# Kernel tuning notes

Hardware: AMD Instinct MI355X
Metric: run time of the kernel (lower is better)

The kernel has to match this reference:

```python
import jax, jax.numpy as jnp
import numpy as np

N_NODES = 50000
N_EDGES = 800000
D_IN = 128
D_OUT = 128


def setup_inputs() -> dict:
    key = jax.random.key(0)
    k_feat, k_src, k_dst, k_ws, k_bs, k_wn = jax.random.split(key, 6)
    feat = jax.random.normal(k_feat, (N_NODES, D_IN), dtype=jnp.float32)
    src = jax.random.randint(k_src, (N_EDGES,), 0, N_NODES, dtype=jnp.int64)
    dst = jax.random.randint(k_dst, (N_EDGES,), 0, N_NODES, dtype=jnp.int64)
    # fc_self: Linear(D_IN, D_OUT, bias=True); fc_neigh: Linear(D_IN, D_OUT, bias=False)
    W_self = jax.random.normal(k_ws, (D_OUT, D_IN), dtype=jnp.float32) * (1.0 / np.sqrt(D_IN))
    b_self = jax.random.normal(k_bs, (D_OUT,), dtype=jnp.float32) * 0.01
    # xavier_uniform with relu gain
    gain = float(np.sqrt(2.0))
    bound = gain * float(np.sqrt(6.0 / (D_IN + D_OUT)))
    W_neigh = jax.random.uniform(k_wn, (D_OUT, D_IN), dtype=jnp.float32, minval=-bound, maxval=bound)
    bias = jnp.zeros((D_OUT,), dtype=jnp.float32)
    return {"feat": feat, "src": src, "dst": dst, "W_self": W_self,
            "b_self": b_self, "W_neigh": W_neigh, "bias": bias}


def reference(feat, src, dst, W_self, b_self, W_neigh, bias):
    # copy_u('h','m') + fn.mean('m','neigh'): gather src feats, mean-reduce by dst.
    # lin_before_mp is False (in_feats == out_feats), so aggregate raw feats first.
    n = feat.shape[0]
    msgs = feat[src]                                             # [E, D_IN]
    neigh_sum = jax.ops.segment_sum(msgs, dst, num_segments=n)   # [N, D_IN]
    deg = jax.ops.segment_sum(jnp.ones(src.shape, feat.dtype), dst, num_segments=n)
    # DGL mean yields 0 for zero-in-degree nodes
    h_neigh = jnp.where(deg[:, None] > 0, neigh_sum / jnp.maximum(deg, 1.0)[:, None], 0.0)
    h_neigh = h_neigh @ W_neigh.T                                # fc_neigh (no bias)
    h_self = feat @ W_self.T + b_self                            # fc_self
    return h_self + h_neigh + bias
```

## Files before the change

kernel.cpp:

```cpp
#include <hip/hip_runtime.h>
#include <hip/hip_fp8.h>

#define N_NODES 50000
#define N_EDGES 800000
#define D 128
#define NBUK 196
#define CAPR 4591
#define CAPP 6400
#define PCHUNK 4096
#define PBLOCKS 196

typedef __bf16 bf16x8 __attribute__((ext_vector_type(8)));
typedef __bf16 bf16x4 __attribute__((ext_vector_type(4)));
typedef float  f32x4  __attribute__((ext_vector_type(4)));
typedef float  f32x2  __attribute__((ext_vector_type(2)));

#if defined(__has_builtin)
#if __has_builtin(__builtin_amdgcn_cvt_pk_f32_fp8) && __has_builtin(__builtin_amdgcn_cvt_pk_fp8_f32)
#define HW_FP8 1
#endif
#endif

#define OFF_GCURSOR   0ull
#define OFF_OFFS      1024ull
#define OFF_PACKED    201216ull
#define OFF_FEAT8     5218816ull
#define OFF_WC16      11618944ull
#define OFF_BIASC     11684480ull

__global__ __launch_bounds__(256)
void partition_kernel(const int* __restrict__ src, const int* __restrict__ dst,
                      int* __restrict__ gcursor, int* __restrict__ packed, int n) {
    __shared__ int lh[NBUK];
    __shared__ int lbase[NBUK];
    const int tid = threadIdx.x;
    const int e0 = blockIdx.x * PCHUNK;
    int d[16], s[16];
    for (int i = tid; i < NBUK; i += 256) lh[i] = 0;
    __syncthreads();
    #pragma unroll
    for (int j = 0; j < 16; ++j) {
        int e = e0 + j * 256 + tid;
        bool ok = e < n;
        d[j] = ok ? dst[e] : -1;
        s[j] = ok ? src[e] : 0;
        if (ok) atomicAdd(&lh[d[j] >> 8], 1);
    }
    __syncthreads();
    for (int i = tid; i < NBUK; i += 256) {
        int c = lh[i];
        lbase[i] = c ? atomicAdd(&gcursor[i], c) : 0;
    }
    __syncthreads();
    for (int i = tid; i < NBUK; i += 256) lh[i] = 0;
    __syncthreads();
    #pragma unroll
    for (int j = 0; j < 16; ++j) {
        if (d[j] >= 0) {
            int b = d[j] >> 8;
            int r = atomicAdd(&lh[b], 1);
            int pos = lbase[b] + r;
            if (pos < CAPR)
                packed[b * CAPP + pos] = ((d[j] & 255) << 16) | s[j];
        }
    }
}

__global__ __launch_bounds__(256)
void mix_kernel(int* __restrict__ packed, const int* __restrict__ gcursor,
                int* __restrict__ offs,
                const float* __restrict__ feat, unsigned char* __restrict__ feat8,
                const float* __restrict__ Ws, const float* __restrict__ Wn,
                const float* __restrict__ b_self, const float* __restrict__ bias,
                __bf16* __restrict__ Wc16, float* __restrict__ biasc) {
    __shared__ int pk[CAPR];
    __shared__ int srt[CAPP];
    __shared__ int lh[256];
    __shared__ int loff[256];
    __shared__ int ws5[5];
    const int tid = threadIdx.x;
    if (blockIdx.x < NBUK) {
        const int lane = tid & 63;
        const int wv = tid >> 6;
        const int b = blockIdx.x;
        const int node0 = b * 256;
        const int ncnt = min(256, N_NODES - node0);
        const int base = b * CAPP;
        const int cnt = min(gcursor[b], CAPR);

        for (int i = tid; i < cnt; i += 256) pk[i] = packed[base + i];
        lh[tid] = 0;
        __syncthreads();
        for (int i = tid; i < cnt; i += 256)
            atomicAdd(&lh[pk[i] >> 16], 1);
        __syncthreads();
        int c  = lh[tid];
        int cp = (c + 7) & ~7;
        int v = cp;
        #pragma unroll
        for (int o = 1; o < 64; o <<= 1) {
            int u = __shfl_up(v, o);
            if (lane >= o) v += u;
        }
        if (lane == 63) ws5[wv] = v;
        __syncthreads();
        if (tid == 0) {
            int r = 0;
            #pragma unroll
            for (int j = 0; j < 4; ++j) { int t = ws5[j]; ws5[j] = r; r += t; }
            ws5[4] = r;
        }
        __syncthreads();
        int ex = ws5[wv] + (v - cp);
        loff[tid] = ex;
        lh[tid] = 0;
        __syncthreads();
        for (int i = tid; i < cnt; i += 256) {
            int p = pk[i];
            int l = p >> 16;
            int r = atomicAdd(&lh[l], 1);
            srt[loff[l] + r] = p & 0xFFFF;
        }
        for (int j = c; j < cp; ++j) srt[ex + j] = N_NODES;
        __syncthreads();
        const int ptot = ws5[4];
        for (int i = tid; i < ptot; i += 256) packed[base + i] = srt[i];
        if (tid < ncnt) offs[node0 + tid] = (ex << 16) | c;
    } else if (blockIdx.x < NBUK + 3125) {
        size_t i = ((size_t)(blockIdx.x - NBUK) * 256 + tid) * 8;
        float4 f0 = *(const float4*)(feat + i);
        float4 f1 = *(const float4*)(feat + i + 4);
#ifdef HW_FP8
        int q0 = __builtin_amdgcn_cvt_pk_fp8_f32(f0.x, f0.y, 0, false);
        q0     = __builtin_amdgcn_cvt_pk_fp8_f32(f0.z, f0.w, q0, true);
        int q1 = __builtin_amdgcn_cvt_pk_fp8_f32(f1.x, f1.y, 0, false);
        q1     = __builtin_amdgcn_cvt_pk_fp8_f32(f1.z, f1.w, q1, true);
        uint2 qq; qq.x = (unsigned)q0; qq.y = (unsigned)q1;
        *(uint2*)(feat8 + i) = qq;
#else
        float fv[8] = {f0.x, f0.y, f0.z, f0.w, f1.x, f1.y, f1.z, f1.w};
        union { unsigned char b[8]; unsigned long long u; } q;
        #pragma unroll
        for (int j = 0; j < 8; ++j) { __hip_fp8_e4m3 e(fv[j]); q.b[j] = e.__x; }
        *(unsigned long long*)(feat8 + i) = q.u;
#endif
    } else if (blockIdx.x < NBUK + 3157) {
        int idx = (blockIdx.x - NBUK - 3125) * 256 + tid;
        int col = idx >> 6;
        int kq  = (idx & 63) * 4;
        const float* srcp = (kq < D) ? (Ws + (size_t)col * D + kq)
                                     : (Wn + (size_t)col * D + (kq - D));
        float4 f = *(const float4*)srcp;
        bf16x4 t;
        t[0]=(__bf16)f.x; t[1]=(__bf16)f.y; t[2]=(__bf16)f.z; t[3]=(__bf16)f.w;
        *(bf16x4*)(Wc16 + (size_t)col * 256 + kq) = t;
    } else {
        if (tid < D) biasc[tid] = b_self[tid] + bias[tid];
        else if (tid < D + 32)
            ((unsigned*)(feat8 + (size_t)N_NODES * D))[tid - 128] = 0u;
    }
}

__device__ __forceinline__
void gemm_tail(__bf16 (*At)[264], const __bf16* __restrict__ Wc16,
               const float* __restrict__ biasc, float* __restrict__ out,
               int node0, int tid) {
    const int wv = tid >> 6;
    const int lane = tid & 63;
    const int m = lane & 15;
    const int quad = lane >> 4;
    const int r0 = (wv & 1) * 32;
    const int c0 = (wv >> 1) * 64;

    f32x4 acc[2][4] = {};
    #pragma unroll
    for (int k0 = 0; k0 < 256; k0 += 32) {
        const int kk = k0 + quad * 8;
        bf16x8 a0 = *(const bf16x8*)&At[r0 + m][kk];
        bf16x8 a1 = *(const bf16x8*)&At[r0 + 16 + m][kk];
        #pragma unroll
        for (int ct = 0; ct < 4; ++ct) {
            int col = c0 + ct * 16 + m;
            bf16x8 b = *(const bf16x8*)(Wc16 + (size_t)col * 256 + kk);
            acc[0][ct] = __builtin_amdgcn_mfma_f32_16x16x32_bf16(a0, b, acc[0][ct], 0, 0, 0);
            acc[1][ct] = __builtin_amdgcn_mfma_f32_16x16x32_bf16(a1, b, acc[1][ct], 0, 0, 0);
        }
    }
    __syncthreads();

    float* Ct = (float*)&At[0][0];
    #pragma unroll
    for (int rt = 0; rt < 2; ++rt) {
        #pragma unroll
        for (int ct = 0; ct < 4; ++ct) {
            int ccol = c0 + ct * 16 + m;
            int crow = r0 + rt * 16 + quad * 4;
            #pragma unroll
            for (int r = 0; r < 4; ++r)
                Ct[(crow + r) * 132 + ccol] = acc[rt][ct][r];
        }
    }
    __syncthreads();
    for (int idx = tid; idx < 64 * 32; idx += 256) {
        int row = idx >> 5;
        int c4 = (idx & 31) * 4;
        int n = node0 + row;
        if (n < N_NODES) {
            float4 v = *(float4*)&Ct[row * 132 + c4];
            float4 bb = *(const float4*)(biasc + c4);
            v.x += bb.x; v.y += bb.y; v.z += bb.z; v.w += bb.w;
            *(float4*)&out[(size_t)n * D + c4] = v;
        }
    }
}

__device__ __forceinline__ float fp8tof_sw(unsigned char b) {
    __hip_fp8_e4m3 t; t.__x = b;
    return (float)t;
}

__global__ __launch_bounds__(256)
void fused_kernel(const float* __restrict__ feat,
                  const unsigned char* __restrict__ feat8,
                  const int* __restrict__ offs,
                  const int* __restrict__ csr,
                  const __bf16* __restrict__ Wc16,
                  const float* __restrict__ biasc,
                  float* __restrict__ out) {
    __shared__ __bf16 At[64][264];
    const int tid = threadIdx.x;
    const int node0 = blockIdx.x * 64;

    for (int idx = tid; idx < 1024; idx += 256) {
        int row = idx >> 4;
        int seg = (idx & 15) * 8;
        int n = node0 + row;
        bf16x8 t = {};
        if (n < N_NODES) {
            const float* p = feat + (size_t)n * D + seg;
            float4 f0 = *(const float4*)p;
            float4 f1 = *(const float4*)(p + 4);
            t[0]=(__bf16)f0.x; t[1]=(__bf16)f0.y; t[2]=(__bf16)f0.z; t[3]=(__bf16)f0.w;
            t[4]=(__bf16)f1.x; t[5]=(__bf16)f1.y; t[6]=(__bf16)f1.z; t[7]=(__bf16)f1.w;
        }
        *(bf16x8*)&At[row][seg] = t;
    }

    {
        const int hw = tid >> 5;
        const int lane = tid & 31;
        const unsigned int* g8 = (const unsigned int*)feat8;
        int ovs[8];
        #pragma unroll
        for (int t = 0; t < 8; ++t) {
            int n = node0 + hw + t * 8;
            ovs[t] = (n < N_NODES) ? offs[n] : 0;
        }
        #pragma unroll
        for (int t = 0; t < 8; ++t) {
            int i = hw + t * 8;
            int n = node0 + i;
            int dg = ovs[t] & 0xFFFF;
            int dgp = (dg + 7) & ~7;
            float a0 = 0.f, a1 = 0.f, a2 = 0.f, a3 = 0.f;
            if (n < N_NODES && dg > 0) {
                const int* lst = csr + (n >> 8) * CAPP + (ovs[t] >> 16);
                for (int j = 0; j < dgp; j += 8) {
                    int s[8]; unsigned int w[8];
                    #pragma unroll
                    for (int q = 0; q < 8; ++q) s[q] = lst[j + q];
                    #pragma unroll
                    for (int q = 0; q < 8; ++q)
                        w[q] = g8[(size_t)s[q] * 32 + lane];
                    #pragma unroll
                    for (int q = 0; q < 8; ++q) {
#ifdef HW_FP8
                        f32x2 lo = __builtin_amdgcn_cvt_pk_f32_fp8((int)w[q], false);
                        f32x2 hi = __builtin_amdgcn_cvt_pk_f32_fp8((int)w[q], true);
                        a0 += lo[0]; a1 += lo[1]; a2 += hi[0]; a3 += hi[1];
#else
                        a0 += fp8tof_sw(w[q] & 0xFF);
                        a1 += fp8tof_sw((w[q] >> 8) & 0xFF);
                        a2 += fp8tof_sw((w[q] >> 16) & 0xFF);
                        a3 += fp8tof_sw(w[q] >> 24);
#endif
                    }
                }
            }
            float sc = dg > 0 ? 1.0f / (float)dg : 0.f;
            bf16x4 hv;
            hv[0] = (__bf16)(a0 * sc); hv[1] = (__bf16)(a1 * sc);
            hv[2] = (__bf16)(a2 * sc); hv[3] = (__bf16)(a3 * sc);
            *(bf16x4*)&At[i][128 + lane * 4] = hv;
        }
    }
    __syncthreads();
    gemm_tail(At, Wc16, biasc, out, node0, tid);
}

extern "C" void kernel_launch(void* const* d_in, const int* in_sizes, int n_in,
                              void* d_out, int out_size, void* d_ws, size_t ws_size,
                              hipStream_t stream) {
    const float* feat    = (const float*)d_in[0];
    const int*   src     = (const int*)d_in[1];
    const int*   dst     = (const int*)d_in[2];
    const float* W_self  = (const float*)d_in[3];
    const float* b_self  = (const float*)d_in[4];
    const float* W_neigh = (const float*)d_in[5];
    const float* bias    = (const float*)d_in[6];
    float* out = (float*)d_out;
    char*  ws  = (char*)d_ws;

    int* gcursor = (int*)(ws + OFF_GCURSOR);
    int* offs    = (int*)(ws + OFF_OFFS);
    int* packed  = (int*)(ws + OFF_PACKED);
    unsigned char* feat8 = (unsigned char*)(ws + OFF_FEAT8);
    __bf16* Wc16 = (__bf16*)(ws + OFF_WC16);
    float* biasc = (float*)(ws + OFF_BIASC);
    const int n_edges = in_sizes[1];

    hipMemsetAsync(gcursor, 0, 1024, stream);
    partition_kernel<<<dim3(PBLOCKS), 256, 0, stream>>>(src, dst, gcursor, packed, n_edges);
    mix_kernel<<<dim3(NBUK + 3158), 256, 0, stream>>>(packed, gcursor, offs,
                                                      feat, feat8, W_self, W_neigh,
                                                      b_self, bias, Wc16, biasc);
    fused_kernel<<<dim3((N_NODES + 63) / 64), 256, 0, stream>>>(
        feat, feat8, offs, packed, Wc16, biasc, out);
}
```

Baseline: 147.1 us.

## Move fp8/weight prep into partition kernel and split gather across half-waves

The fp8 feature quantization and weight/bias packing now run in the same launch as the edge partition, and the local CSR sort becomes its own small kernel. The goal is to overlap the bandwidth-heavy conversion with the atomic-bound partition and keep the sort kernel light on shared memory so it occupies the GPU better. In the gather, each full wave now handles one node, with the two half-waves taking alternate neighbours. Neighbour indices are read as int4 vectors, 16 per iteration, and the two halves are combined with a cross-lane shuffle. This gives more memory parallelism per node but spends half the lanes idle on the write-back and adds shuffles.

```diff
diff --git a/kernel.cpp b/kernel.cpp
--- a/kernel.cpp
+++ b/kernel.cpp
@@ -29,105 +29,48 @@
 #define OFF_BIASC     11684480ull
 
 __global__ __launch_bounds__(256)
-void partition_kernel(const int* __restrict__ src, const int* __restrict__ dst,
-                      int* __restrict__ gcursor, int* __restrict__ packed, int n) {
+void prep_kernel(const int* __restrict__ src, const int* __restrict__ dst,
+                 int* __restrict__ gcursor, int* __restrict__ packed, int n,
+                 const float* __restrict__ feat, unsigned char* __restrict__ feat8,
+                 const float* __restrict__ Ws, const float* __restrict__ Wn,
+                 const float* __restrict__ b_self, const float* __restrict__ bias,
+                 __bf16* __restrict__ Wc16, float* __restrict__ biasc) {
     __shared__ int lh[NBUK];
     __shared__ int lbase[NBUK];
     const int tid = threadIdx.x;
-    const int e0 = blockIdx.x * PCHUNK;
-    int d[16], s[16];
-    for (int i = tid; i < NBUK; i += 256) lh[i] = 0;
-    __syncthreads();
-    #pragma unroll
-    for (int j = 0; j < 16; ++j) {
-        int e = e0 + j * 256 + tid;
-        bool ok = e < n;
-        d[j] = ok ? dst[e] : -1;
-        s[j] = ok ? src[e] : 0;
-        if (ok) atomicAdd(&lh[d[j] >> 8], 1);
-    }
-    __syncthreads();
-    for (int i = tid; i < NBUK; i += 256) {
-        int c = lh[i];
-        lbase[i] = c ? atomicAdd(&gcursor[i], c) : 0;
-    }
-    __syncthreads();
-    for (int i = tid; i < NBUK; i += 256) lh[i] = 0;
-    __syncthreads();
-    #pragma unroll
-    for (int j = 0; j < 16; ++j) {
-        if (d[j] >= 0) {
-            int b = d[j] >> 8;
-            int r = atomicAdd(&lh[b], 1);
-            int pos = lbase[b] + r;
-            if (pos < CAPR)
-                packed[b * CAPP + pos] = ((d[j] & 255) << 16) | s[j];
-        }
-    }
-}
-
-__global__ __launch_bounds__(256)
-void mix_kernel(int* __restrict__ packed, const int* __restrict__ gcursor,
-                int* __restrict__ offs,
-                const float* __restrict__ feat, unsigned char* __restrict__ feat8,
-                const float* __restrict__ Ws, const float* __restrict__ Wn,
-                const float* __restrict__ b_self, const float* __restrict__ bias,
-                __bf16* __restrict__ Wc16, float* __restrict__ biasc) {
-    __shared__ int pk[CAPR];
-    __shared__ int srt[CAPP];
-    __shared__ int lh[256];
-    __shared__ int loff[256];
-    __shared__ int ws5[5];
-    const int tid = threadIdx.x;
-    if (blockIdx.x < NBUK) {
-        const int lane = tid & 63;
-        const int wv = tid >> 6;
-        const int b = blockIdx.x;
-        const int node0 = b * 256;
-        const int ncnt = min(256, N_NODES - node0);
-        const int base = b * CAPP;
-        const int cnt = min(gcursor[b], CAPR);
-
-        for (int i = tid; i < cnt; i += 256) pk[i] = packed[base + i];
-        lh[tid] = 0;
+    if (blockIdx.x < PBLOCKS) {
+        const int e0 = blockIdx.x * PCHUNK;
+        int d[16], s[16];
+        for (int i = tid; i < NBUK; i += 256) lh[i] = 0;
         __syncthreads();
-        for (int i = tid; i < cnt; i += 256)
-            atomicAdd(&lh[pk[i] >> 16], 1);
+        #pragma unroll
+        for (int j = 0; j < 16; ++j) {
+            int e = e0 + j * 256 + tid;
+            bool ok = e < n;
+            d[j] = ok ? dst[e] : -1;
+            s[j] = ok ? src[e] : 0;
+            if (ok) atomicAdd(&lh[d[j] >> 8], 1);
+        }
         __syncthreads();
-        int c  = lh[tid];
-        int cp = (c + 7) & ~7;
-        int v = cp;
-        #pragma unroll
-        for (int o = 1; o < 64; o <<= 1) {
-            int u = __shfl_up(v, o);
-            if (lane >= o) v += u;
-        }
-        if (lane == 63) ws5[wv] = v;
+        for (int i = tid; i < NBUK; i += 256) {
+            int c = lh[i];
+            lbase[i] = c ? atomicAdd(&gcursor[i], c) : 0;
+        }
         __syncthreads();
-        if (tid == 0) {
-            int r = 0;
-            #pragma unroll
-            for (int j = 0; j < 4; ++j) { int t = ws5[j]; ws5[j] = r; r += t; }
-            ws5[4] = r;
-        }
+        for (int i = tid; i < NBUK; i += 256) lh[i] = 0;
         __syncthreads();
-        int ex = ws5[wv] + (v - cp);
-        loff[tid] = ex;
-        lh[tid] = 0;
-        __syncthreads();
-        for (int i = tid; i < cnt; i += 256) {
-            int p = pk[i];
-            int l = p >> 16;
-            int r = atomicAdd(&lh[l], 1);
-            srt[loff[l] + r] = p & 0xFFFF;
-        }
-        for (int j = c; j < cp; ++j) srt[ex + j] = N_NODES;
-        __syncthreads();
-        const int ptot = ws5[4];
-        for (int i = tid; i < ptot; i += 256) packed[base + i] = srt[i];
-        if (tid < ncnt) offs[node0 + tid] = (ex << 16) | c;
-    } else if (blockIdx.x < NBUK + 3125) {
-        size_t i = ((size_t)(blockIdx.x - NBUK) * 256 + tid) * 8;
+        #pragma unroll
+        for (int j = 0; j < 16; ++j) {
+            if (d[j] >= 0) {
+                int b = d[j] >> 8;
+                int r = atomicAdd(&lh[b], 1);
+                int pos = lbase[b] + r;
+                if (pos < CAPR)
+                    packed[b * CAPP + pos] = ((d[j] & 255) << 16) | s[j];
+            }
+        }
+    } else if (blockIdx.x < PBLOCKS + 3125) {
+        size_t i = ((size_t)(blockIdx.x - PBLOCKS) * 256 + tid) * 8;
         float4 f0 = *(const float4*)(feat + i);
         float4 f1 = *(const float4*)(feat + i + 4);
 #ifdef HW_FP8
@@ -144,8 +87,8 @@
         for (int j = 0; j < 8; ++j) { __hip_fp8_e4m3 e(fv[j]); q.b[j] = e.__x; }
         *(unsigned long long*)(feat8 + i) = q.u;
 #endif
-    } else if (blockIdx.x < NBUK + 3157) {
-        int idx = (blockIdx.x - NBUK - 3125) * 256 + tid;
+    } else if (blockIdx.x < PBLOCKS + 3157) {
+        int idx = (blockIdx.x - PBLOCKS - 3125) * 256 + tid;
         int col = idx >> 6;
         int kq  = (idx & 63) * 4;
         const float* srcp = (kq < D) ? (Ws + (size_t)col * D + kq)
@@ -161,62 +104,79 @@
     }
 }
 
-__device__ __forceinline__
-void gemm_tail(__bf16 (*At)[264], const __bf16* __restrict__ Wc16,
-               const float* __restrict__ biasc, float* __restrict__ out,
-               int node0, int tid) {
+__global__ __launch_bounds__(256)
+void csr_local_kernel(int* __restrict__ packed, const int* __restrict__ gcursor,
+                      int* __restrict__ offs) {
+    __shared__ int pk[CAPR];
+    __shared__ int srt[CAPP];
+    __shared__ int lh[256];
+    __shared__ int loff[256];
+    __shared__ int ws5[5];
+    const int tid = threadIdx.x;
+    const int lane = tid & 63;
     const int wv = tid >> 6;
-    const int lane = tid & 63;
-    const int m = lane & 15;
-    const int quad = lane >> 4;
-    const int r0 = (wv & 1) * 32;
-    const int c0 = (wv >> 1) * 64;
-
-    f32x4 acc[2][4] = {};
+    const int b = blockIdx.x;
+    const int node0 = b * 256;
+    const int ncnt = min(256, N_NODES - node0);
+    const int base = b * CAPP;
+    const int cnt = min(gcursor[b], CAPR);
+
+    for (int i = tid; i < cnt; i += 256) pk[i] = packed[base + i];
+    lh[tid] = 0;
+    __syncthreads();
+    for (int i = tid; i < cnt; i += 256)
+        atomicAdd(&lh[pk[i] >> 16], 1);
+    __syncthreads();
+    int c  = lh[tid];
+    int cp = (c + 7) & ~7;
+    int v = cp;
     #pragma unroll
-    for (int k0 = 0; k0 < 256; k0 += 32) {
-        const int kk = k0 + quad * 8;
-        bf16x8 a0 = *(const bf16x8*)&At[r0 + m][kk];
-        bf16x8 a1 = *(const bf16x8*)&At[r0 + 16 + m][kk];
-        #pragma unroll
-        for (int ct = 0; ct < 4; ++ct) {
-            int col = c0 + ct * 16 + m;
-            bf16x8 b = *(const bf16x8*)(Wc16 + (size_t)col * 256 + kk);
-            acc[0][ct] = __builtin_amdgcn_mfma_f32_16x16x32_bf16(a0, b, acc[0][ct], 0, 0, 0);
-            acc[1][ct] = __builtin_amdgcn_mfma_f32_16x16x32_bf16(a1, b, acc[1][ct], 0, 0, 0);
-        }
-    }
-    __syncthreads();
-
-    float* Ct = (float*)&At[0][0];
-    #pragma unroll
-    for (int rt = 0; rt < 2; ++rt) {
-        #pragma unroll
-        for (int ct = 0; ct < 4; ++ct) {
-            int ccol = c0 + ct * 16 + m;
-            int crow = r0 + rt * 16 + quad * 4;
-            #pragma unroll
-            for (int r = 0; r < 4; ++r)
-                Ct[(crow + r) * 132 + ccol] = acc[rt][ct][r];
-        }
-    }
-    __syncthreads();
-    for (int idx = tid; idx < 64 * 32; idx += 256) {
-        int row = idx >> 5;
-        int c4 = (idx & 31) * 4;
-        int n = node0 + row;
-        if (n < N_NODES) {
-            float4 v = *(float4*)&Ct[row * 132 + c4];
-            float4 bb = *(const float4*)(biasc + c4);
-            v.x += bb.x; v.y += bb.y; v.z += bb.z; v.w += bb.w;
-            *(float4*)&out[(size_t)n * D + c4] = v;
-        }
-    }
+    for (int o = 1; o < 64; o <<= 1) {
+        int u = __shfl_up(v, o);
+        if (lane >= o) v += u;
+    }
+    if (lane == 63) ws5[wv] = v;
+    __syncthreads();
+    if (tid == 0) {
+        int r = 0;
+        #pragma unroll
+        for (int j = 0; j < 4; ++j) { int t = ws5[j]; ws5[j] = r; r += t; }
+        ws5[4] = r;
+    }
+    __syncthreads();
+    int ex = ws5[wv] + (v - cp);
+    loff[tid] = ex;
+    lh[tid] = 0;
+    __syncthreads();
+    for (int i = tid; i < cnt; i += 256) {
+        int p = pk[i];
+        int l = p >> 16;
+        int r = atomicAdd(&lh[l], 1);
+        srt[loff[l] + r] = p & 0xFFFF;
+    }
+    for (int j = c; j < cp; ++j) srt[ex + j] = N_NODES;
+    __syncthreads();
+    const int ptot = ws5[4];
+    for (int i = tid; i < ptot; i += 256) packed[base + i] = srt[i];
+    if (tid < ncnt) offs[node0 + tid] = (ex << 16) | c;
 }
 
 __device__ __forceinline__ float fp8tof_sw(unsigned char b) {
     __hip_fp8_e4m3 t; t.__x = b;
     return (float)t;
+}
+__device__ __forceinline__ void dec_add(unsigned int w, float& a0, float& a1,
+                                        float& a2, float& a3) {
+#ifdef HW_FP8
+    f32x2 lo = __builtin_amdgcn_cvt_pk_f32_fp8((int)w, false);
+    f32x2 hi = __builtin_amdgcn_cvt_pk_f32_fp8((int)w, true);
+    a0 += lo[0]; a1 += lo[1]; a2 += hi[0]; a3 += hi[1];
+#else
+    a0 += fp8tof_sw(w & 0xFF);
+    a1 += fp8tof_sw((w >> 8) & 0xFF);
+    a2 += fp8tof_sw((w >> 16) & 0xFF);
+    a3 += fp8tof_sw(w >> 24);
+#endif
 }
 
 __global__ __launch_bounds__(256)
@@ -247,55 +207,112 @@
     }
 
     {
-        const int hw = tid >> 5;
-        const int lane = tid & 31;
+        const int wv = tid >> 6;
+        const int lane = tid & 63;
+        const int hi = lane >> 5;
+        const int l32 = lane & 31;
         const unsigned int* g8 = (const unsigned int*)feat8;
-        int ovs[8];
-        #pragma unroll
-        for (int t = 0; t < 8; ++t) {
-            int n = node0 + hw + t * 8;
-            ovs[t] = (n < N_NODES) ? offs[n] : 0;
-        }
-        #pragma unroll
-        for (int t = 0; t < 8; ++t) {
-            int i = hw + t * 8;
-            int n = node0 + i;
-            int dg = ovs[t] & 0xFFFF;
-            int dgp = (dg + 7) & ~7;
+        for (int t = 0; t < 16; ++t) {
+            const int i = wv + t * 4;
+            const int n = node0 + i;
+            const int ov = (n < N_NODES) ? offs[n] : 0;
+            const int dg = ov & 0xFFFF;
+            const int dgp = (dg + 7) & ~7;
             float a0 = 0.f, a1 = 0.f, a2 = 0.f, a3 = 0.f;
-            if (n < N_NODES && dg > 0) {
-                const int* lst = csr + (n >> 8) * CAPP + (ovs[t] >> 16);
-                for (int j = 0; j < dgp; j += 8) {
-                    int s[8]; unsigned int w[8];
+            if (dg > 0) {
+                const int* lst = csr + (n >> 8) * CAPP + (ov >> 16);
+                int j = 0;
+                for (; j + 16 <= dgp; j += 16) {
+                    int4 A = *(const int4*)(lst + j);
+                    int4 B = *(const int4*)(lst + j + 4);
+                    int4 C = *(const int4*)(lst + j + 8);
+                    int4 E = *(const int4*)(lst + j + 12);
+                    unsigned int w[8];
+                    w[0] = g8[(size_t)(hi ? A.y : A.x) * 32 + l32];
+                    w[1] = g8[(size_t)(hi ? A.w : A.z) * 32 + l32];
+                    w[2] = g8[(size_t)(hi ? B.y : B.x) * 32 + l32];
+                    w[3] = g8[(size_t)(hi ? B.w : B.z) * 32 + l32];
+                    w[4] = g8[(size_t)(hi ? C.y : C.x) * 32 + l32];
+                    w[5] = g8[(size_t)(hi ? C.w : C.z) * 32 + l32];
+                    w[6] = g8[(size_t)(hi ? E.y : E.x) * 32 + l32];
+                    w[7] = g8[(size_t)(hi ? E.w : E.z) * 32 + l32];
                     #pragma unroll
-                    for (int q = 0; q < 8; ++q) s[q] = lst[j + q];
+                    for (int q = 0; q < 8; ++q) dec_add(w[q], a0, a1, a2, a3);
+                }
+                if (j < dgp) {
+                    int4 A = *(const int4*)(lst + j);
+                    int4 B = *(const int4*)(lst + j + 4);
+                    unsigned int w[4];
+                    w[0] = g8[(size_t)(hi ? A.y : A.x) * 32 + l32];
+                    w[1] = g8[(size_t)(hi ? A.w : A.z) * 32 + l32];
+                    w[2] = g8[(size_t)(hi ? B.y : B.x) * 32 + l32];
+                    w[3] = g8[(size_t)(hi ? B.w : B.z) * 32 + l32];
                     #pragma unroll
-                    for (int q = 0; q < 8; ++q)
-                        w[q] = g8[(size_t)s[q] * 32 + lane];
-                    #pragma unroll
-                    for (int q = 0; q < 8; ++q) {
-#ifdef HW_FP8
-                        f32x2 lo = __builtin_amdgcn_cvt_pk_f32_fp8((int)w[q], false);
-                        f32x2 hi = __builtin_amdgcn_cvt_pk_f32_fp8((int)w[q], true);
-                        a0 += lo[0]; a1 += lo[1]; a2 += hi[0]; a3 += hi[1];
-#else
-                        a0 += fp8tof_sw(w[q] & 0xFF);
-                        a1 += fp8tof_sw((w[q] >> 8) & 0xFF);
-                        a2 += fp8tof_sw((w[q] >> 16) & 0xFF);
-                        a3 += fp8tof_sw(w[q] >> 24);
-#endif
-                    }
+                    for (int q = 0; q < 4; ++q) dec_add(w[q], a0, a1, a2, a3);
                 }
             }
+            a0 += __shfl_xor(a0, 32);
+            a1 += __shfl_xor(a1, 32);
+            a2 += __shfl_xor(a2, 32);
+            a3 += __shfl_xor(a3, 32);
             float sc = dg > 0 ? 1.0f / (float)dg : 0.f;
-            bf16x4 hv;
-            hv[0] = (__bf16)(a0 * sc); hv[1] = (__bf16)(a1 * sc);
-            hv[2] = (__bf16)(a2 * sc); hv[3] = (__bf16)(a3 * sc);
-            *(bf16x4*)&At[i][128 + lane * 4] = hv;
-        }
-    }
-    __syncthreads();
-    gemm_tail(At, Wc16, biasc, out, node0, tid);
+            if (hi == 0) {
+                bf16x4 hv;
+                hv[0] = (__bf16)(a0 * sc); hv[1] = (__bf16)(a1 * sc);
+                hv[2] = (__bf16)(a2 * sc); hv[3] = (__bf16)(a3 * sc);
+                *(bf16x4*)&At[i][128 + l32 * 4] = hv;
+            }
+        }
+    }
+    __syncthreads();
+
+    const int wv = tid >> 6;
+    const int lane = tid & 63;
+    const int m = lane & 15;
+    const int quad = lane >> 4;
+    const int r0 = (wv & 1) * 32;
+    const int c0 = (wv >> 1) * 64;
+
+    f32x4 acc[2][4] = {};
+    #pragma unroll
+    for (int k0 = 0; k0 < 256; k0 += 32) {
+        const int kk = k0 + quad * 8;
+        bf16x8 a0 = *(const bf16x8*)&At[r0 + m][kk];
+        bf16x8 a1 = *(const bf16x8*)&At[r0 + 16 + m][kk];
+        #pragma unroll
+        for (int ct = 0; ct < 4; ++ct) {
+            int col = c0 + ct * 16 + m;
+            bf16x8 b = *(const bf16x8*)(Wc16 + (size_t)col * 256 + kk);
+            acc[0][ct] = __builtin_amdgcn_mfma_f32_16x16x32_bf16(a0, b, acc[0][ct], 0, 0, 0);
+            acc[1][ct] = __builtin_amdgcn_mfma_f32_16x16x32_bf16(a1, b, acc[1][ct], 0, 0, 0);
+        }
+    }
+    __syncthreads();
+
+    float* Ct = (float*)&At[0][0];
+    #pragma unroll
+    for (int rt = 0; rt < 2; ++rt) {
+        #pragma unroll
+        for (int ct = 0; ct < 4; ++ct) {
+            int ccol = c0 + ct * 16 + m;
+            int crow = r0 + rt * 16 + quad * 4;
+            #pragma unroll
+            for (int r = 0; r < 4; ++r)
+                Ct[(crow + r) * 132 + ccol] = acc[rt][ct][r];
+        }
+    }
+    __syncthreads();
+    for (int idx = tid; idx < 64 * 32; idx += 256) {
+        int row = idx >> 5;
+        int c4 = (idx & 31) * 4;
+        int n = node0 + row;
+        if (n < N_NODES) {
+            float4 v = *(float4*)&Ct[row * 132 + c4];
+            float4 bb = *(const float4*)(biasc + c4);
+            v.x += bb.x; v.y += bb.y; v.z += bb.z; v.w += bb.w;
+            *(float4*)&out[(size_t)n * D + c4] = v;
+        }
+    }
 }
 
 extern "C" void kernel_launch(void* const* d_in, const int* in_sizes, int n_in,
@@ -320,10 +337,10 @@
     const int n_edges = in_sizes[1];
 
     hipMemsetAsync(gcursor, 0, 1024, stream);
-    partition_kernel<<<dim3(PBLOCKS), 256, 0, stream>>>(src, dst, gcursor, packed, n_edges);
-    mix_kernel<<<dim3(NBUK + 3158), 256, 0, stream>>>(packed, gcursor, offs,
-                                                      feat, feat8, W_self, W_neigh,
-                                                      b_self, bias, Wc16, biasc);
+    prep_kernel<<<dim3(PBLOCKS + 3158), 256, 0, stream>>>(
+        src, dst, gcursor, packed, n_edges,
+        feat, feat8, W_self, W_neigh, b_self, bias, Wc16, biasc);
+    csr_local_kernel<<<dim3(NBUK), 256, 0, stream>>>(packed, gcursor, offs);
     fused_kernel<<<dim3((N_NODES + 63) / 64), 256, 0, stream>>>(
         feat, feat8, offs, packed, Wc16, biasc, out);
 }
```

Result: slower. 156.2 us (+6.1%).
